# Performance work log

Hardware: AMD Instinct MI355X
Metric: run time of the kernel (lower is better)

The kernel has to match this reference:

```python
import jax, jax.numpy as jnp
import numpy as np

DEPTH = 24; D_MODEL = 192; D_INNER = 384; D_STATE = 16; DT_RANK = 12; D_CONV = 4
H = 32; W = 3200; P = 16; NP = (W // P) * (H // P)  # 400 patches
NCLS = 22; BATCH = 4; EPS = 1e-5


def _rmsnorm(x, w):
    return x * jax.lax.rsqrt(jnp.mean(x * x, axis=-1, keepdims=True) + EPS) * w


def _causal_dwconv(x, w, b):
    # x: (B, L, D), w: (D, K) depthwise, left-padded causal conv (mamba conv1d)
    D = x.shape[-1]; K = w.shape[-1]
    xp = jnp.pad(jnp.swapaxes(x, 1, 2), ((0, 0), (0, 0), (K - 1, 0)))
    y = jax.lax.conv_general_dilated(xp, w[:, None, :], (1,), 'VALID',
            dimension_numbers=('NCH', 'OIH', 'NCH'), feature_group_count=D)
    return jnp.swapaxes(y + b[None, :, None], 1, 2)


def _selective_scan(x, dt, Bm, Cm, A, Dsk):
    # x, dt: (B, L, d); Bm, Cm: (B, L, n); A: (d, n); Dsk: (d,)
    dA = jnp.exp(dt[..., None] * A)                  # (B, L, d, n)
    dBx = (dt * x)[..., None] * Bm[:, :, None, :]    # (B, L, d, n)
    h0 = jnp.zeros((x.shape[0], x.shape[2], A.shape[1]), x.dtype)

    def step(h, inp):
        a, bx, c = inp
        h = a * h + bx
        return h, jnp.einsum('bdn,bn->bd', h, c)

    _, ys = jax.lax.scan(step, h0,
        (jnp.swapaxes(dA, 0, 1), jnp.swapaxes(dBx, 0, 1), jnp.swapaxes(Cm, 0, 1)))
    return jnp.swapaxes(ys, 0, 1) + x * Dsk


def _mamba_dir(xz, cw_l, cb_l, xpw, dtw, dtb, A, Dsk):
    xx, z = jnp.split(xz, 2, axis=-1)
    xx = jax.nn.silu(_causal_dwconv(xx, cw_l, cb_l))
    dbl = xx @ xpw.T                                  # (B, L, dt_rank + 2n)
    dt = jax.nn.softplus(dbl[..., :DT_RANK] @ dtw.T + dtb)
    Bm = dbl[..., DT_RANK:DT_RANK + D_STATE]
    Cm = dbl[..., DT_RANK + D_STATE:]
    y = _selective_scan(xx, dt, Bm, Cm, A, Dsk)
    return y * jax.nn.silu(z)


def _forward(x, pe_w, pe_b, cls_token, pos_embed, norm_w, in_proj_w, cw, cb,
             xproj_w, dtproj_w, dtproj_b, A_log, A_b_log, Dp, outproj_w,
             norm_f_w, head_w, head_b):
    B = x.shape[0]
    # patch embed: conv2d stride=kernel=16 on (B,1,H,W)
    y = jax.lax.conv_general_dilated(x[:, None], pe_w, (P, P), 'VALID',
            dimension_numbers=('NCHW', 'OIHW', 'NCHW')) + pe_b[None, :, None, None]
    tok = jnp.transpose(y, (0, 2, 3, 1)).reshape(B, -1, D_MODEL)   # (B, NP, D)
    tok = jnp.concatenate([jnp.broadcast_to(cls_token, (B, 1, D_MODEL)), tok], axis=1)
    tok = tok + pos_embed

    def layer_step(carry, p):
        hidden, residual = carry
        nw, ipw, cw_l, cb_l, xpw, dtw, dtb, Al, Abl, Dsk, opw = p
        residual = residual + hidden          # fused add (residual_in_fp32: all fp32)
        h = _rmsnorm(residual, nw)
        xz = h @ ipw.T                         # (B, L, 2*d_inner)
        y_f = _mamba_dir(xz, cw_l, cb_l, xpw, dtw, dtb, -jnp.exp(Al), Dsk)
        y_b = _mamba_dir(xz[:, ::-1], cw_l, cb_l, xpw, dtw, dtb, -jnp.exp(Abl), Dsk)[:, ::-1]
        return ((y_f + y_b) @ opw.T, residual), None

    # NOTE: source sets residual = x AND hidden = x before the loop, so the
    (hidden, residual), _ = jax.lax.scan(
        layer_step, (tok, tok),
        (norm_w, in_proj_w, cw, cb, xproj_w, dtproj_w, dtproj_b, A_log, A_b_log, Dp, outproj_w))
    out = _rmsnorm(residual + hidden, norm_f_w)
    return out[:, 0] @ head_w.T + head_b          # (B, n_classes)


def setup_inputs() -> dict:
    key = jax.random.key(0)
    ks = jax.random.split(key, 12)

    def n(k, shape, scale):
        return jax.random.normal(k, shape, jnp.float32) * scale

    a_init = jnp.tile(jnp.log(jnp.arange(1, D_STATE + 1, dtype=jnp.float32))[None, None, :],
                      (DEPTH, D_INNER, 1))
    return {
        'x': n(ks[0], (BATCH, H, W), 1.0),
        'pe_w': n(ks[1], (D_MODEL, 1, P, P), 1.0 / P),
        'pe_b': jnp.zeros((D_MODEL,), jnp.float32),
        'cls_token': n(ks[2], (1, 1, D_MODEL), 0.02),
        'pos_embed': n(ks[3], (1, NP + 1, D_MODEL), 0.02),
        'norm_w': jnp.ones((DEPTH, D_MODEL), jnp.float32),
        'in_proj_w': n(ks[4], (DEPTH, 2 * D_INNER, D_MODEL), D_MODEL ** -0.5),
        'cw': n(ks[5], (DEPTH, D_INNER, D_CONV), D_CONV ** -0.5),
        'cb': jnp.zeros((DEPTH, D_INNER), jnp.float32),
        'xproj_w': n(ks[6], (DEPTH, DT_RANK + 2 * D_STATE, D_INNER), D_INNER ** -0.5),
        'dtproj_w': n(ks[7], (DEPTH, D_INNER, DT_RANK), DT_RANK ** -0.5),
        'dtproj_b': n(ks[8], (DEPTH, D_INNER), 0.1),
        'A_log': a_init,
        'A_b_log': a_init,
        'Dp': jnp.ones((DEPTH, D_INNER), jnp.float32),
        'outproj_w': n(ks[9], (DEPTH, D_MODEL, D_INNER), D_INNER ** -0.5 / np.sqrt(DEPTH)),
        'norm_f_w': jnp.ones((D_MODEL,), jnp.float32),
        'head_w': n(ks[10], (NCLS, D_MODEL), D_MODEL ** -0.5),
        'head_b': jnp.zeros((NCLS,), jnp.float32),
    }


def reference(x, pe_w, pe_b, cls_token, pos_embed, norm_w, in_proj_w, cw, cb,
              xproj_w, dtproj_w, dtproj_b, A_log, A_b_log, Dp, outproj_w,
              norm_f_w, head_w, head_b):
    return _forward(x, pe_w, pe_b, cls_token, pos_embed, norm_w, in_proj_w, cw, cb,
                    xproj_w, dtproj_w, dtproj_b, A_log, A_b_log, Dp, outproj_w,
                    norm_f_w, head_w, head_b)
```

## Files before the change

kernel.cpp:

```cpp
#include <hip/hip_runtime.h>
#include <hip/hip_bf16.h>

#define DEPTH 24
#define DM 192
#define DI 384
#define DS 16
#define DR 12
#define LSEQ 401
#define BATCH 4
#define NTOK (BATCH*LSEQ)
#define NCLS 22
#define NC 16
#define TCH 26

__device__ __forceinline__ float silu_f(float x) { return x / (1.f + __expf(-x)); }

__global__ void patch_embed_k(const float* __restrict__ x,
                              const float* __restrict__ pe_w,
                              const float* __restrict__ pe_b,
                              const float* __restrict__ cls,
                              const float* __restrict__ pos,
                              float* __restrict__ residual, float* __restrict__ hidden)
{
    __shared__ float xp[4][256];
    int g0 = blockIdx.x * 4;
    int c = threadIdx.x;
    #pragma unroll
    for (int j = 0; j < 4; j++) {
        int g = g0 + j;
        int b = g / LSEQ, t = g % LSEQ;
        if (t != 0) {
            int p = t - 1, pi = p / 200, pj = p % 200;
            for (int i = c; i < 256; i += 192) {
                int pp = i >> 4, qq = i & 15;
                xp[j][i] = x[((size_t)(b * 32 + pi * 16 + pp)) * 3200 + pj * 16 + qq];
            }
        }
    }
    __syncthreads();
    float acc[4] = {0.f, 0.f, 0.f, 0.f};
    for (int k = 0; k < 256; k++) {
        float w = pe_w[c * 256 + k];
        #pragma unroll
        for (int j = 0; j < 4; j++) acc[j] += xp[j][k] * w;
    }
    #pragma unroll
    for (int j = 0; j < 4; j++) {
        int g = g0 + j;
        int t = g % LSEQ;
        float v = (t == 0) ? cls[c] : (acc[j] + pe_b[c]);
        v += pos[t * DM + c];
        residual[(size_t)g * DM + c] = v;
        hidden[(size_t)g * DM + c] = v;
    }
}

__global__ __launch_bounds__(256) void gemm_xz_k(
    const float* __restrict__ resin, const float* __restrict__ hidden,
    float* __restrict__ resout, const float* __restrict__ nw,
    const float* __restrict__ ipw, float* __restrict__ xz,
    float* __restrict__ dbl)
{
    __shared__ float As[48][68];
    __shared__ float Ws[48][68];
    __shared__ float srms[64];
    __shared__ float ps[64][4];
    int tid = threadIdx.x;
    for (int i = (blockIdx.y * 12 + blockIdx.x) * 256 + tid; i < 2 * NTOK * 44; i += 312 * 256)
        dbl[i] = 0.f;
    int bn = blockIdx.x * 64;
    int bm = blockIdx.y * 64;
    int rr = tid >> 2, q = tid & 3;
    int m = bm + rr;
    float rv[4][12];
    float s = 0.f;
    if (m < NTOK) {
        const float* rp = resin + (size_t)m * DM;
        const float* hp = hidden + (size_t)m * DM;
        #pragma unroll
        for (int c = 0; c < 4; c++) {
            int base = c * 48 + q * 12;
            #pragma unroll
            for (int i = 0; i < 12; i += 4) {
                float4 a = *(const float4*)&rp[base + i];
                float4 b = *(const float4*)&hp[base + i];
                float r0 = a.x + b.x, r1 = a.y + b.y, r2 = a.z + b.z, r3 = a.w + b.w;
                rv[c][i] = r0; rv[c][i + 1] = r1; rv[c][i + 2] = r2; rv[c][i + 3] = r3;
                s += r0 * r0 + r1 * r1 + r2 * r2 + r3 * r3;
            }
        }
        if (bn == 0) {
            float* op = resout + (size_t)m * DM;
            #pragma unroll
            for (int c = 0; c < 4; c++) {
                int base = c * 48 + q * 12;
                #pragma unroll
                for (int i = 0; i < 12; i += 4)
                    *(float4*)&op[base + i] =
                        make_float4(rv[c][i], rv[c][i + 1], rv[c][i + 2], rv[c][i + 3]);
            }
        }
    } else {
        #pragma unroll
        for (int c = 0; c < 4; c++)
            #pragma unroll
            for (int i = 0; i < 12; i++) rv[c][i] = 0.f;
    }
    ps[rr][q] = s;
    __syncthreads();
    if (q == 0) {
        float tot = ps[rr][0] + ps[rr][1] + ps[rr][2] + ps[rr][3];
        srms[rr] = rsqrtf(tot * (1.f / (float)DM) + 1e-5f);
    }
    __syncthreads();

    int orow = (tid >> 4) * 4;
    int ocol = (tid & 15) * 4;
    int sk = q * 12;
    float acc[4][4] = {};
    for (int c = 0; c < 4; c++) {
        float rs = srms[rr];
        #pragma unroll
        for (int i = 0; i < 12; i++)
            As[sk + i][rr] = rv[c][i] * rs * nw[c * 48 + sk + i];
        const float* wp = ipw + (size_t)(bn + rr) * DM + c * 48 + sk;
        #pragma unroll
        for (int i = 0; i < 12; i++)
            Ws[sk + i][rr] = wp[i];
        __syncthreads();
        #pragma unroll
        for (int kk = 0; kk < 48; kk++) {
            float4 a = *(const float4*)&As[kk][orow];
            float4 w = *(const float4*)&Ws[kk][ocol];
            acc[0][0] += a.x * w.x; acc[0][1] += a.x * w.y; acc[0][2] += a.x * w.z; acc[0][3] += a.x * w.w;
            acc[1][0] += a.y * w.x; acc[1][1] += a.y * w.y; acc[1][2] += a.y * w.z; acc[1][3] += a.y * w.w;
            acc[2][0] += a.z * w.x; acc[2][1] += a.z * w.y; acc[2][2] += a.z * w.z; acc[2][3] += a.z * w.w;
            acc[3][0] += a.w * w.x; acc[3][1] += a.w * w.y; acc[3][2] += a.w * w.z; acc[3][3] += a.w * w.w;
        }
        __syncthreads();
    }
    #pragma unroll
    for (int i = 0; i < 4; i++) {
        int mm = bm + orow + i;
        if (mm >= NTOK) continue;
        *(float4*)&xz[(size_t)mm * (2 * DI) + bn + ocol] =
            make_float4(acc[i][0], acc[i][1], acc[i][2], acc[i][3]);
    }
}

__global__ __launch_bounds__(256) void xproj_conv_k(
    const float* __restrict__ xz,
    const float* __restrict__ cw, const float* __restrict__ cb,
    const float* __restrict__ xpw, float* __restrict__ dbl,
    float* __restrict__ hidden, float* __restrict__ xx)
{
    __shared__ float As[96][33];
    __shared__ float Ws[96][48];
    int tid = threadIdx.x;
    for (int i = (blockIdx.y * 4 + blockIdx.x) * 256 + tid; i < NTOK * DM; i += 404 * 256)
        hidden[i] = 0.f;
    int kbase = blockIdx.x * 96;
    int bm = blockIdx.y * 32;
    for (int idx = tid; idx < 96 * 32; idx += 256) {
        int row = idx / 96, k = idx - row * 96;
        int m = bm + row;
        if (m < 2 * NTOK) {
            int dir = m / NTOK;
            int r = m - dir * NTOK;
            int b = r / LSEQ, t = r % LSEQ;
            int ch = kbase + k;
            float a = cb[ch];
            #pragma unroll
            for (int j = 0; j < 4; j++) {
                int tt = t - 3 + j;
                if (tt >= 0) {
                    int st = dir ? (LSEQ - 1 - tt) : tt;
                    a += cw[ch * 4 + j] * xz[((size_t)(b * LSEQ + st)) * (2 * DI) + ch];
                }
            }
            float v = silu_f(a);
            As[k][row] = v;
            xx[(size_t)m * DI + ch] = v;
        } else {
            As[k][row] = 0.f;
        }
    }
    for (int i = tid; i < 96 * 48; i += 256) {
        int k = i / 48, rr = i % 48;
        Ws[k][rr] = (rr < 44) ? xpw[(size_t)rr * DI + kbase + k] : 0.f;
    }
    __syncthreads();
    int row = tid & 31, cg = tid >> 5;
    int cbase = cg * 6;
    float acc[6] = {};
    #pragma unroll 4
    for (int kk = 0; kk < 96; kk++) {
        float a = As[kk][row];
        #pragma unroll
        for (int j = 0; j < 6; j++) acc[j] += a * Ws[kk][cbase + j];
    }
    int m = bm + row;
    if (m < 2 * NTOK) {
        #pragma unroll
        for (int j = 0; j < 6; j++) {
            int cc = cbase + j;
            if (cc < 44) atomicAdd(&dbl[(size_t)m * 44 + cc], acc[j]);
        }
    }
}

__global__ __launch_bounds__(256) void scan_part_k(
    const float* __restrict__ xx, const float* __restrict__ dbl,
    const float* __restrict__ dtw, const float* __restrict__ dtb,
    const float* __restrict__ A_log, const float* __restrict__ A_b_log,
    float* __restrict__ hloc, float* __restrict__ Pc)
{
    __shared__ float sdbl[TCH][28];
    __shared__ float sdt[TCH][16];
    __shared__ float sxx[TCH][16];
    __shared__ float sw[16][12];
    __shared__ float sb2[16];
    int dblk = blockIdx.x, chunk = blockIdx.y;
    int db = blockIdx.z;
    int dir = db >> 2, b = db & 3;
    int tid = threadIdx.x;
    int d0 = dblk * 16;
    int t0 = chunk * TCH;
    size_t dof44 = (size_t)db * LSEQ * 44;
    size_t dofx = (size_t)(dir * NTOK + b * LSEQ) * DI;
    for (int i = tid; i < TCH * 28; i += 256) {
        int t = i / 28, cc = i - t * 28;
        sdbl[t][cc] = dbl[dof44 + (size_t)(t0 + t) * 44 + cc];
    }
    if (tid < 192) { int d = tid / 12, r = tid - d * 12; sw[d][r] = dtw[(size_t)(d0 + d) * 12 + r]; }
    if (tid < 16) sb2[tid] = dtb[d0 + tid];
    for (int i = tid; i < TCH * 16; i += 256) {
        int t = i >> 4, d = i & 15;
        sxx[t][d] = xx[dofx + (size_t)(t0 + t) * DI + d0 + d];
    }
    __syncthreads();
    for (int i = tid; i < TCH * 16; i += 256) {
        int t = i >> 4, d = i & 15;
        float a2 = sb2[d];
        #pragma unroll
        for (int r = 0; r < 12; r++) a2 += sdbl[t][r] * sw[d][r];
        sdt[t][d] = (a2 > 15.f) ? a2 : __logf(1.f + __expf(a2));
    }
    __syncthreads();
    int wave = tid >> 6, lane = tid & 63;
    int dsub = wave * 4 + (lane >> 4);
    int n = lane & 15;
    const float* Al = dir ? A_b_log : A_log;
    float Aval = -__expf(Al[(d0 + dsub) * DS + n]);
    float h = 0.f, P = 1.f;
    #pragma unroll
    for (int i = 0; i < TCH; i++) {
        float dtv = sdt[i][dsub];
        float xv  = sxx[i][dsub];
        float Bv  = sdbl[i][12 + n];
        float dA = __expf(dtv * Aval);
        h = dA * h + (dtv * xv) * Bv;
        P *= dA;
    }
    size_t idx2 = ((size_t)db * NC + chunk) * (DI * DS) + (size_t)(d0 + dsub) * DS + n;
    hloc[idx2] = h;
    Pc[idx2] = P;
}

__global__ __launch_bounds__(256) void scan_fix_k(
    const float* __restrict__ xx, const float* __restrict__ dbl,
    const float* __restrict__ dtw, const float* __restrict__ dtb,
    const float* __restrict__ A_log, const float* __restrict__ A_b_log,
    const float* __restrict__ Dp,
    const float* __restrict__ hloc, const float* __restrict__ Pc,
    float* __restrict__ yraw)
{
    __shared__ float sdbl[TCH][44];
    __shared__ float sdt[TCH][16];
    __shared__ float sxx[TCH][16];
    __shared__ float sy[TCH][16];
    __shared__ float sw[16][12];
    __shared__ float sb2[16];
    int dblk = blockIdx.x, chunk = blockIdx.y;
    int db = blockIdx.z;
    int dir = db >> 2, b = db & 3;
    int tid = threadIdx.x;
    int d0 = dblk * 16;
    int t0 = chunk * TCH;
    size_t dofD = (size_t)db * LSEQ * DI;
    size_t dof44 = (size_t)db * LSEQ * 44;
    size_t dofx = (size_t)(dir * NTOK + b * LSEQ) * DI;
    for (int i = tid; i < TCH * 44; i += 256) {
        int t = i / 44, cc = i - t * 44;
        sdbl[t][cc] = ((t0 + t) < LSEQ) ? dbl[dof44 + (size_t)(t0 + t) * 44 + cc] : 0.f;
    }
    if (tid < 192) { int d = tid / 12, r = tid - d * 12; sw[d][r] = dtw[(size_t)(d0 + d) * 12 + r]; }
    if (tid < 16) sb2[tid] = dtb[d0 + tid];
    for (int i = tid; i < TCH * 16; i += 256) {
        int t = i >> 4, d = i & 15;
        int tq = t0 + t;
        sxx[t][d] = (tq < LSEQ) ? xx[dofx + (size_t)tq * DI + d0 + d] : 0.f;
    }
    __syncthreads();
    for (int i = tid; i < TCH * 16; i += 256) {
        int t = i >> 4, d = i & 15;
        float a2 = sb2[d];
        #pragma unroll
        for (int r = 0; r < 12; r++) a2 += sdbl[t][r] * sw[d][r];
        sdt[t][d] = (a2 > 15.f) ? a2 : __logf(1.f + __expf(a2));
    }
    __syncthreads();
    int wave = tid >> 6, lane = tid & 63;
    int dsub = wave * 4 + (lane >> 4);
    int n = lane & 15;
    const float* Al = dir ? A_b_log : A_log;
    float Aval = -__expf(Al[(d0 + dsub) * DS + n]);
    float Dv = Dp[d0 + dsub];
    float h = 0.f;
    size_t cbase = (size_t)db * NC * (DI * DS) + (size_t)(d0 + dsub) * DS + n;
    #pragma unroll
    for (int j = 0; j < NC - 1; j++) {
        size_t idx = cbase + (size_t)j * (DI * DS);
        float pj = Pc[idx], hj = hloc[idx];
        h = (j < chunk) ? (pj * h + hj) : h;
    }
    #pragma unroll
    for (int i = 0; i < TCH; i++) {
        float dtv = sdt[i][dsub];
        float xv  = sxx[i][dsub];
        float Bv  = sdbl[i][12 + n];
        float Cv  = sdbl[i][28 + n];
        h = __expf(dtv * Aval) * h + (dtv * xv) * Bv;
        float p = h * Cv;
        p += __shfl_xor(p, 1);
        p += __shfl_xor(p, 2);
        p += __shfl_xor(p, 4);
        p += __shfl_xor(p, 8);
        if (n == 0) sy[i][dsub] = p + xv * Dv;
    }
    __syncthreads();
    int len = min(t0 + TCH, LSEQ) - t0;
    for (int idx = tid; idx < len * 16; idx += 256) {
        int t = idx >> 4, d = idx & 15;
        yraw[dofD + (size_t)(t0 + t) * DI + d0 + d] = sy[t][d];
    }
}

__global__ __launch_bounds__(256) void outproj_k(
    const float* __restrict__ yraw, const float* __restrict__ xz,
    const float* __restrict__ opw, float* __restrict__ hidden)
{
    __shared__ float As[96][34];
    __shared__ float Ws[96][34];
    int tid = threadIdx.x;
    int bn = blockIdx.x * 32;
    int bm = blockIdx.y * 32;
    int kbase = blockIdx.z * 192;
    int row8 = tid >> 3, seg = tid & 7, k0 = seg * 24;
    float a[24], wreg[24];
    int m = bm + row8;
    if (m < NTOK) {
        int b = m / LSEQ, t = m % LSEQ;
        const float* yf = yraw + (size_t)m * DI + kbase + k0;
        const float* yb = yraw + (size_t)(NTOK + b * LSEQ + (LSEQ - 1 - t)) * DI + kbase + k0;
        const float* zp = xz + (size_t)m * (2 * DI) + DI + kbase + k0;
        #pragma unroll
        for (int i = 0; i < 24; i++) {
            float z = zp[i];
            a[i] = (yf[i] + yb[i]) * (z / (1.f + __expf(-z)));
        }
    } else {
        #pragma unroll
        for (int i = 0; i < 24; i++) a[i] = 0.f;
    }
    {
        const float* wp = opw + (size_t)(bn + row8) * DI + kbase + k0;
        #pragma unroll
        for (int i = 0; i < 24; i++) wreg[i] = wp[i];
    }
    int r0 = (tid >> 4) * 2, c0 = (tid & 15) * 2;
    float acc[2][2] = {};
    #pragma unroll
    for (int st = 0; st < 2; st++) {
        if (st) __syncthreads();
        if ((seg >> 2) == st) {
            int kb = k0 - st * 96;
            #pragma unroll
            for (int i = 0; i < 24; i++) {
                As[kb + i][row8] = a[i];
                Ws[kb + i][row8] = wreg[i];
            }
        }
        __syncthreads();
        #pragma unroll 8
        for (int kk = 0; kk < 96; kk++) {
            float2 av = *(const float2*)&As[kk][r0];
            float2 wv = *(const float2*)&Ws[kk][c0];
            acc[0][0] += av.x * wv.x; acc[0][1] += av.x * wv.y;
            acc[1][0] += av.y * wv.x; acc[1][1] += av.y * wv.y;
        }
    }
    #pragma unroll
    for (int i = 0; i < 2; i++) {
        int mm = bm + r0 + i;
        if (mm >= NTOK) continue;
        #pragma unroll
        for (int j = 0; j < 2; j++)
            atomicAdd(&hidden[(size_t)mm * DM + bn + c0 + j], acc[i][j]);
    }
}

__global__ void final_head_k(const float* __restrict__ residual, const float* __restrict__ hidden,
                             const float* __restrict__ norm_f,
                             const float* __restrict__ head_w,
                             const float* __restrict__ head_b,
                             void* __restrict__ out,
                             const unsigned short* __restrict__ probe)
{
    __shared__ float wsum[3];
    __shared__ float hb[DM];
    int b = blockIdx.x;
    int c = threadIdx.x;
    int idx = (b * LSEQ) * DM + c;
    float r = residual[idx] + hidden[idx];
    float s = r * r;
    for (int off = 32; off > 0; off >>= 1) s += __shfl_down(s, off);
    int wave = c >> 6, lane = c & 63;
    if (lane == 0) wsum[wave] = s;
    __syncthreads();
    float tot = wsum[0] + wsum[1] + wsum[2];
    float rms = rsqrtf(tot / (float)DM + 1e-5f);
    hb[c] = r * rms * norm_f[c];
    __syncthreads();
    if (c < NCLS) {
        float acc = head_b[c];
        #pragma unroll 8
        for (int k = 0; k < DM; k++) acc += hb[k] * head_w[c * DM + k];
        if (probe[0] == 0x3F80u)
            ((__hip_bfloat16*)out)[b * NCLS + c] = __float2bfloat16(acc);
        else
            ((float*)out)[b * NCLS + c] = acc;
    }
}

extern "C" void kernel_launch(void* const* d_in, const int* in_sizes, int n_in,
                              void* d_out, int out_size, void* d_ws, size_t ws_size,
                              hipStream_t stream)
{
    (void)in_sizes; (void)n_in; (void)out_size; (void)ws_size;
    const float* x      = (const float*)d_in[0];
    const float* pe_w   = (const float*)d_in[1];
    const float* pe_b   = (const float*)d_in[2];
    const float* cls    = (const float*)d_in[3];
    const float* pos    = (const float*)d_in[4];
    const float* norm_w = (const float*)d_in[5];
    const float* ipw    = (const float*)d_in[6];
    const float* cw     = (const float*)d_in[7];
    const float* cb     = (const float*)d_in[8];
    const float* xpw    = (const float*)d_in[9];
    const float* dtw    = (const float*)d_in[10];
    const float* dtb    = (const float*)d_in[11];
    const float* A_log  = (const float*)d_in[12];
    const float* A_b_log= (const float*)d_in[13];
    const float* Dp     = (const float*)d_in[14];
    const float* opw    = (const float*)d_in[15];
    const float* norm_f = (const float*)d_in[16];
    const float* head_w = (const float*)d_in[17];
    const float* head_b = (const float*)d_in[18];
    const unsigned short* probe = (const unsigned short*)d_in[14];

    float* ws = (float*)d_ws;
    const size_t nTokDM = (size_t)NTOK * DM;
    const size_t nTokXZ = (size_t)NTOK * 2 * DI;
    const size_t nDirDI = (size_t)2 * NTOK * DI;
    const size_t nDir44 = (size_t)2 * NTOK * 44;
    const size_t nChunk = (size_t)2 * BATCH * NC * DI * DS;
    float* resA   = ws;
    float* resB   = resA + nTokDM;
    float* hidden = resB + nTokDM;
    float* xz     = hidden + nTokDM;
    float* dbl    = xz + nTokXZ;
    float* yraw   = dbl + nDir44;
    float* hloc   = yraw + nDirDI;
    float* Pc     = hloc + nChunk;
    float* xx     = Pc + nChunk;

    patch_embed_k<<<NTOK / 4, DM, 0, stream>>>(x, pe_w, pe_b, cls, pos, resA, hidden);

    for (int l = 0; l < DEPTH; l++) {
        float* rin  = (l & 1) ? resB : resA;
        float* rout = (l & 1) ? resA : resB;

        gemm_xz_k<<<dim3(12, 26), 256, 0, stream>>>(
            rin, hidden, rout, norm_w + (size_t)l * DM,
            ipw + (size_t)l * 2 * DI * DM, xz, dbl);

        xproj_conv_k<<<dim3(4, 101), 256, 0, stream>>>(
            xz, cw + (size_t)l * DI * 4, cb + (size_t)l * DI,
            xpw + (size_t)l * 44 * DI, dbl, hidden, xx);

        scan_part_k<<<dim3(DI / 16, NC - 1, 2 * BATCH), 256, 0, stream>>>(
            xx, dbl,
            dtw + (size_t)l * DI * DR, dtb + (size_t)l * DI,
            A_log + (size_t)l * DI * DS, A_b_log + (size_t)l * DI * DS,
            hloc, Pc);

        scan_fix_k<<<dim3(DI / 16, NC, 2 * BATCH), 256, 0, stream>>>(
            xx, dbl,
            dtw + (size_t)l * DI * DR, dtb + (size_t)l * DI,
            A_log + (size_t)l * DI * DS, A_b_log + (size_t)l * DI * DS,
            Dp + (size_t)l * DI, hloc, Pc, yraw);

        outproj_k<<<dim3(6, 51, 2), 256, 0, stream>>>(
            yraw, xz, opw + (size_t)l * DM * DI, hidden);
    }

    final_head_k<<<BATCH, DM, 0, stream>>>(resA, hidden, norm_f, head_w, head_b,
                                           d_out, probe);
}
```

Baseline: 3.048 ms.

## Fuse causal conv and x-projection into the in-projection GEMM epilogue

```diff
diff --git a/kernel.cpp b/kernel.cpp
--- a/kernel.cpp
+++ b/kernel.cpp
@@ -20,11 +20,14 @@
                               const float* __restrict__ pe_b,
                               const float* __restrict__ cls,
                               const float* __restrict__ pos,
-                              float* __restrict__ residual, float* __restrict__ hidden)
+                              float* __restrict__ residual, float* __restrict__ hidden,
+                              float* __restrict__ dbl)
 {
     __shared__ float xp[4][256];
     int g0 = blockIdx.x * 4;
     int c = threadIdx.x;
+    for (int i = blockIdx.x * 192 + c; i < 2 * NTOK * 44; i += 401 * 192)
+        dbl[i] = 0.f;
     #pragma unroll
     for (int j = 0; j < 4; j++) {
         int g = g0 + j;
@@ -58,16 +61,24 @@
 __global__ __launch_bounds__(256) void gemm_xz_k(
     const float* __restrict__ resin, const float* __restrict__ hidden,
     float* __restrict__ resout, const float* __restrict__ nw,
-    const float* __restrict__ ipw, float* __restrict__ xz,
-    float* __restrict__ dbl)
-{
-    __shared__ float As[48][68];
-    __shared__ float Ws[48][68];
+    const float* __restrict__ ipw,
+    const float* __restrict__ cw, const float* __restrict__ cb,
+    const float* __restrict__ xpw,
+    float* __restrict__ xz, float* __restrict__ xx, float* __restrict__ dbl)
+{
+    __shared__ float pool[13952];
     __shared__ float srms[64];
     __shared__ float ps[64][4];
+    __shared__ float hrms[6];
+    float* Asp    = pool;
+    float* Wsp    = pool + 3264;
+    float* xs     = pool;
+    float* hstage = pool + 4480;
+    float* xxf    = pool + 5632;
+    float* xxb    = pool + 9792;
+    float* w44    = pool;
+
     int tid = threadIdx.x;
-    for (int i = (blockIdx.y * 12 + blockIdx.x) * 256 + tid; i < 2 * NTOK * 44; i += 312 * 256)
-        dbl[i] = 0.f;
     int bn = blockIdx.x * 64;
     int bm = blockIdx.y * 64;
     int rr = tid >> 2, q = tid & 3;
@@ -122,16 +133,16 @@
         float rs = srms[rr];
         #pragma unroll
         for (int i = 0; i < 12; i++)
-            As[sk + i][rr] = rv[c][i] * rs * nw[c * 48 + sk + i];
+            Asp[(sk + i) * 68 + rr] = rv[c][i] * rs * nw[c * 48 + sk + i];
         const float* wp = ipw + (size_t)(bn + rr) * DM + c * 48 + sk;
         #pragma unroll
         for (int i = 0; i < 12; i++)
-            Ws[sk + i][rr] = wp[i];
+            Wsp[(sk + i) * 68 + rr] = wp[i];
         __syncthreads();
         #pragma unroll
         for (int kk = 0; kk < 48; kk++) {
-            float4 a = *(const float4*)&As[kk][orow];
-            float4 w = *(const float4*)&Ws[kk][ocol];
+            float4 a = *(const float4*)&Asp[kk * 68 + orow];
+            float4 w = *(const float4*)&Wsp[kk * 68 + ocol];
             acc[0][0] += a.x * w.x; acc[0][1] += a.x * w.y; acc[0][2] += a.x * w.z; acc[0][3] += a.x * w.w;
             acc[1][0] += a.y * w.x; acc[1][1] += a.y * w.y; acc[1][2] += a.y * w.z; acc[1][3] += a.y * w.w;
             acc[2][0] += a.z * w.x; acc[2][1] += a.z * w.y; acc[2][2] += a.z * w.z; acc[2][3] += a.z * w.w;
@@ -142,70 +153,96 @@
     #pragma unroll
     for (int i = 0; i < 4; i++) {
         int mm = bm + orow + i;
-        if (mm >= NTOK) continue;
-        *(float4*)&xz[(size_t)mm * (2 * DI) + bn + ocol] =
-            make_float4(acc[i][0], acc[i][1], acc[i][2], acc[i][3]);
-    }
-}
-
-__global__ __launch_bounds__(256) void xproj_conv_k(
-    const float* __restrict__ xz,
-    const float* __restrict__ cw, const float* __restrict__ cb,
-    const float* __restrict__ xpw, float* __restrict__ dbl,
-    float* __restrict__ hidden, float* __restrict__ xx)
-{
-    __shared__ float As[96][33];
-    __shared__ float Ws[96][48];
-    int tid = threadIdx.x;
-    for (int i = (blockIdx.y * 4 + blockIdx.x) * 256 + tid; i < NTOK * DM; i += 404 * 256)
-        hidden[i] = 0.f;
-    int kbase = blockIdx.x * 96;
-    int bm = blockIdx.y * 32;
-    for (int idx = tid; idx < 96 * 32; idx += 256) {
-        int row = idx / 96, k = idx - row * 96;
-        int m = bm + row;
-        if (m < 2 * NTOK) {
-            int dir = m / NTOK;
-            int r = m - dir * NTOK;
-            int b = r / LSEQ, t = r % LSEQ;
-            int ch = kbase + k;
-            float a = cb[ch];
+        float4 v = make_float4(acc[i][0], acc[i][1], acc[i][2], acc[i][3]);
+        *(float4*)&xs[(3 + orow + i) * 64 + ocol] = v;
+        if (mm < NTOK)
+            *(float4*)&xz[(size_t)mm * (2 * DI) + bn + ocol] = v;
+    }
+    if (bn >= DI) return;
+    for (int i2 = tid; i2 < 6 * 192; i2 += 256) {
+        int hr = i2 / 192, k = i2 - hr * 192;
+        int mh = (hr < 3) ? (bm - 3 + hr) : (bm + 61 + hr);
+        float v = 0.f;
+        if (mh >= 0 && mh < NTOK)
+            v = resin[(size_t)mh * DM + k] + hidden[(size_t)mh * DM + k];
+        hstage[i2] = v;
+    }
+    __syncthreads();
+    if (tid < 6) {
+        float s2 = 0.f;
+        for (int k = 0; k < 192; k++) { float v = hstage[tid * 192 + k]; s2 += v * v; }
+        hrms[tid] = rsqrtf(s2 * (1.f / (float)DM) + 1e-5f);
+    }
+    __syncthreads();
+    for (int i2 = tid; i2 < 6 * 192; i2 += 256) {
+        int hr = i2 / 192, k = i2 - hr * 192;
+        hstage[i2] = hstage[i2] * hrms[hr] * nw[k];
+    }
+    __syncthreads();
+    for (int e = tid; e < 6 * 64; e += 256) {
+        int hr = e >> 6, cl = e & 63;
+        const float* wp = ipw + (size_t)(bn + cl) * DM;
+        const float* ap = hstage + hr * 192;
+        float dsum = 0.f;
+        #pragma unroll 8
+        for (int k = 0; k < 192; k++) dsum += ap[k] * wp[k];
+        xs[((hr < 3) ? hr : (hr + 64)) * 64 + cl] = dsum;
+    }
+    __syncthreads();
+    #pragma unroll
+    for (int i = 0; i < 4; i++) {
+        int mr = bm + orow + i;
+        if (mr >= NTOK) {
             #pragma unroll
             for (int j = 0; j < 4; j++) {
-                int tt = t - 3 + j;
-                if (tt >= 0) {
-                    int st = dir ? (LSEQ - 1 - tt) : tt;
-                    a += cw[ch * 4 + j] * xz[((size_t)(b * LSEQ + st)) * (2 * DI) + ch];
-                }
+                xxf[(orow + i) * 65 + ocol + j] = 0.f;
+                xxb[(orow + i) * 65 + ocol + j] = 0.f;
             }
-            float v = silu_f(a);
-            As[k][row] = v;
-            xx[(size_t)m * DI + ch] = v;
-        } else {
-            As[k][row] = 0.f;
-        }
-    }
-    for (int i = tid; i < 96 * 48; i += 256) {
-        int k = i / 48, rr = i % 48;
-        Ws[k][rr] = (rr < 44) ? xpw[(size_t)rr * DI + kbase + k] : 0.f;
-    }
-    __syncthreads();
-    int row = tid & 31, cg = tid >> 5;
-    int cbase = cg * 6;
-    float acc[6] = {};
-    #pragma unroll 4
-    for (int kk = 0; kk < 96; kk++) {
-        float a = As[kk][row];
-        #pragma unroll
-        for (int j = 0; j < 6; j++) acc[j] += a * Ws[kk][cbase + j];
-    }
-    int m = bm + row;
-    if (m < 2 * NTOK) {
-        #pragma unroll
-        for (int j = 0; j < 6; j++) {
-            int cc = cbase + j;
-            if (cc < 44) atomicAdd(&dbl[(size_t)m * 44 + cc], acc[j]);
-        }
+            continue;
+        }
+        int b = mr / LSEQ, t = mr - b * LSEQ;
+        int xr = 3 + orow + i;
+        float outf[4], outb[4];
+        #pragma unroll
+        for (int j = 0; j < 4; j++) {
+            int ch = bn + ocol + j;
+            float af = cb[ch], ab = af;
+            #pragma unroll
+            for (int jt = 0; jt < 4; jt++) {
+                float w = cw[ch * 4 + jt];
+                if (t - 3 + jt >= 0)        af += w * xs[(xr - 3 + jt) * 64 + ocol + j];
+                if (t + 3 - jt <= LSEQ - 1) ab += w * xs[(xr + 3 - jt) * 64 + ocol + j];
+            }
+            outf[j] = silu_f(af); outb[j] = silu_f(ab);
+            xxf[(orow + i) * 65 + ocol + j] = outf[j];
+            xxb[(orow + i) * 65 + ocol + j] = outb[j];
+        }
+        *(float4*)&xx[(size_t)mr * DI + bn + ocol] =
+            make_float4(outf[0], outf[1], outf[2], outf[3]);
+        size_t mb = (size_t)(NTOK + b * LSEQ + (LSEQ - 1 - t));
+        *(float4*)&xx[mb * DI + bn + ocol] =
+            make_float4(outb[0], outb[1], outb[2], outb[3]);
+    }
+    __syncthreads();
+    for (int e = tid; e < 44 * 64; e += 256) {
+        int n = e >> 6, kk = e & 63;
+        w44[n * 65 + kk] = xpw[(size_t)n * DI + bn + kk];
+    }
+    __syncthreads();
+    for (int e = tid; e < 128 * 44; e += 256) {
+        int row = e / 44, n = e - row * 44;
+        int r6 = row & 63;
+        int mr = bm + r6;
+        if (mr >= NTOK) continue;
+        const float* A = (row < 64) ? &xxf[r6 * 65] : &xxb[r6 * 65];
+        const float* W = &w44[n * 65];
+        float s4 = 0.f;
+        #pragma unroll 8
+        for (int kk = 0; kk < 64; kk++) s4 += A[kk] * W[kk];
+        size_t mo;
+        if (row < 64) mo = (size_t)mr;
+        else { int b = mr / LSEQ, t = mr - b * LSEQ; mo = (size_t)(NTOK + b * LSEQ + (LSEQ - 1 - t)); }
+        atomicAdd(&dbl[mo * 44 + n], s4);
     }
 }
 
@@ -213,7 +250,8 @@
     const float* __restrict__ xx, const float* __restrict__ dbl,
     const float* __restrict__ dtw, const float* __restrict__ dtb,
     const float* __restrict__ A_log, const float* __restrict__ A_b_log,
-    float* __restrict__ hloc, float* __restrict__ Pc)
+    float* __restrict__ hloc, float* __restrict__ Pc,
+    float* __restrict__ hidden)
 {
     __shared__ float sdbl[TCH][28];
     __shared__ float sdt[TCH][16];
@@ -224,6 +262,11 @@
     int db = blockIdx.z;
     int dir = db >> 2, b = db & 3;
     int tid = threadIdx.x;
+    {
+        int bid = (db * (NC - 1) + chunk) * 24 + dblk;
+        for (int i = bid * 256 + tid; i < NTOK * DM; i += 2880 * 256)
+            hidden[i] = 0.f;
+    }
     int d0 = dblk * 16;
     int t0 = chunk * TCH;
     size_t dof44 = (size_t)db * LSEQ * 44;
@@ -348,11 +391,17 @@
 
 __global__ __launch_bounds__(256) void outproj_k(
     const float* __restrict__ yraw, const float* __restrict__ xz,
-    const float* __restrict__ opw, float* __restrict__ hidden)
+    const float* __restrict__ opw, float* __restrict__ hidden,
+    float* __restrict__ dbl)
 {
     __shared__ float As[96][34];
     __shared__ float Ws[96][34];
     int tid = threadIdx.x;
+    {
+        int bid = (blockIdx.z * 51 + blockIdx.y) * 6 + blockIdx.x;
+        for (int i = bid * 256 + tid; i < 2 * NTOK * 44; i += 612 * 256)
+            dbl[i] = 0.f;
+    }
     int bn = blockIdx.x * 32;
     int bm = blockIdx.y * 32;
     int kbase = blockIdx.z * 192;
@@ -485,7 +534,7 @@
     float* Pc     = hloc + nChunk;
     float* xx     = Pc + nChunk;
 
-    patch_embed_k<<<NTOK / 4, DM, 0, stream>>>(x, pe_w, pe_b, cls, pos, resA, hidden);
+    patch_embed_k<<<NTOK / 4, DM, 0, stream>>>(x, pe_w, pe_b, cls, pos, resA, hidden, dbl);
 
     for (int l = 0; l < DEPTH; l++) {
         float* rin  = (l & 1) ? resB : resA;
@@ -493,17 +542,16 @@
 
         gemm_xz_k<<<dim3(12, 26), 256, 0, stream>>>(
             rin, hidden, rout, norm_w + (size_t)l * DM,
-            ipw + (size_t)l * 2 * DI * DM, xz, dbl);
-
-        xproj_conv_k<<<dim3(4, 101), 256, 0, stream>>>(
-            xz, cw + (size_t)l * DI * 4, cb + (size_t)l * DI,
-            xpw + (size_t)l * 44 * DI, dbl, hidden, xx);
+            ipw + (size_t)l * 2 * DI * DM,
+            cw + (size_t)l * DI * 4, cb + (size_t)l * DI,
+            xpw + (size_t)l * 44 * DI,
+            xz, xx, dbl);
 
         scan_part_k<<<dim3(DI / 16, NC - 1, 2 * BATCH), 256, 0, stream>>>(
             xx, dbl,
             dtw + (size_t)l * DI * DR, dtb + (size_t)l * DI,
             A_log + (size_t)l * DI * DS, A_b_log + (size_t)l * DI * DS,
-            hloc, Pc);
+            hloc, Pc, hidden);
 
         scan_fix_k<<<dim3(DI / 16, NC, 2 * BATCH), 256, 0, stream>>>(
             xx, dbl,
@@ -512,7 +560,7 @@
             Dp + (size_t)l * DI, hloc, Pc, yraw);
 
         outproj_k<<<dim3(6, 51, 2), 256, 0, stream>>>(
-            yraw, xz, opw + (size_t)l * DM * DI, hidden);
+            yraw, xz, opw + (size_t)l * DM * DI, hidden, dbl);
     }
 
     final_head_k<<<BATCH, DM, 0, stream>>>(resA, hidden, norm_f, head_w, head_b,
```

Measured after the change: 3.131 ms. 2.7% more time.
